# Kernel optimization log

Hardware: AMD Instinct MI355X
Metric: run time of the kernel (lower is better)

## Reference

```python
import jax, jax.numpy as jnp
import numpy as np

B, H, W, C, NH = 128, 14, 14, 768, 12
HD = C // NH  # 64
L = 2 * H - 1  # 27, rel pos table length


def setup_inputs() -> dict:
    key = jax.random.key(0)
    ks = jax.random.split(key, 6)
    return {
        "hidden_states": jax.random.normal(ks[0], (B, H, W, C), jnp.float32),
        "w_qkv": jax.random.normal(ks[1], (C, 3 * C), jnp.float32) * 0.02,
        "b_qkv": jnp.zeros((3 * C,), jnp.float32),
        "rel_pos_h": jax.random.normal(ks[2], (L, HD), jnp.float32) * 0.02,
        "rel_pos_w": jax.random.normal(ks[3], (L, HD), jnp.float32) * 0.02,
        "w_proj": jax.random.normal(ks[4], (C, C), jnp.float32) * 0.02,
        "b_proj": jnp.zeros((C,), jnp.float32),
    }


def _rel_table(size, rel_pos):
    # q_size == k_size -> coords = q - k + (size - 1), pure gather (no resize)
    coords = jnp.arange(size)[:, None] - jnp.arange(size)[None, :] + (size - 1)
    return rel_pos[coords]  # (size, size, HD)


def reference(hidden_states, w_qkv, b_qkv, rel_pos_h, rel_pos_w, w_proj, b_proj):
    scale = HD ** -0.5
    x = hidden_states.reshape(B, H * W, C)
    qkv = x @ w_qkv + b_qkv                                    # (B, HW, 3C)
    qkv = qkv.reshape(B, H * W, 3, NH, HD)
    qkv = jnp.transpose(qkv, (2, 0, 3, 1, 4)).reshape(3, B * NH, H * W, HD)
    q, k, v = qkv[0], qkv[1], qkv[2]                           # (B*NH, HW, HD)

    attn = jnp.einsum('bqd,bkd->bqk', q * scale, k)            # (B*NH, HW, HW)

    Rh = _rel_table(H, rel_pos_h)                              # (H, H, HD)
    Rw = _rel_table(W, rel_pos_w)                              # (W, W, HD)
    qr = q.reshape(B * NH, H, W, HD)
    rel_h = jnp.einsum('bhwc,hkc->bhwk', qr, Rh)               # (B*NH, H, W, H)
    rel_w = jnp.einsum('bhwc,wkc->bhwk', qr, Rw)               # (B*NH, H, W, W)

    attn = attn.reshape(B * NH, H, W, H, W)
    attn = attn + rel_h[..., :, None] + rel_w[..., None, :]
    attn = attn.reshape(B * NH, H * W, H * W)
    attn = jax.nn.softmax(attn, axis=-1)

    out = attn @ v                                             # (B*NH, HW, HD)
    out = out.reshape(B, NH, H, W, HD)
    out = jnp.transpose(out, (0, 2, 3, 1, 4)).reshape(B, H, W, C)
    return out @ w_proj + b_proj
```

## Files before the change

kernel.cpp:

```cpp
#include <hip/hip_runtime.h>

typedef __bf16 bf16_t;
typedef __bf16 bf16x4 __attribute__((ext_vector_type(4)));
typedef __bf16 bf16x8 __attribute__((ext_vector_type(8)));
typedef float floatx4 __attribute__((ext_vector_type(4)));

#define B_    128
#define H_    14
#define HW_   196
#define C_    768
#define NH_   12
#define HD_   64
#define M_    25088
#define NQKV_ 2304
#define KDIM_ 768
#define BK_   64
#define NKT_  12
#define VPAD_ 208
#define RSTR  72
#define QSTR  104
#define PSTR  232

__device__ __forceinline__ void async_cp16(const void* g, void* l) {
    __builtin_amdgcn_global_load_lds((const __attribute__((address_space(1))) void*)g,
                                     (__attribute__((address_space(3))) void*)l, 16, 0, 0);
}

__global__ __launch_bounds__(256) void cast_x_kernel(const float* __restrict__ in,
                                                     bf16_t* __restrict__ out) {
    size_t i = ((size_t)blockIdx.x * 256 + threadIdx.x) * 8;
    float4 a = *(const float4*)(in + i);
    float4 b = *(const float4*)(in + i + 4);
    bf16x8 v;
    v[0] = (bf16_t)a.x; v[1] = (bf16_t)a.y; v[2] = (bf16_t)a.z; v[3] = (bf16_t)a.w;
    v[4] = (bf16_t)b.x; v[5] = (bf16_t)b.y; v[6] = (bf16_t)b.z; v[7] = (bf16_t)b.w;
    *(bf16x8*)(out + i) = v;
}

__global__ __launch_bounds__(256) void zero_vpad_kernel(bf16_t* __restrict__ vtb) {
    int row = blockIdx.x * 256 + threadIdx.x;
    if (row < B_ * NH_ * HD_) {
        bf16_t* p = vtb + (size_t)row * VPAD_ + HW_;
        #pragma unroll
        for (int i = 0; i < 12; i++) p[i] = (bf16_t)0.f;
    }
}

__global__ __launch_bounds__(256) void transpose_cast_kernel(const float* __restrict__ in,
                                                             bf16_t* __restrict__ out,
                                                             int rows, int cols) {
    __shared__ float tile[32][33];
    int c0 = blockIdx.x * 32, r0 = blockIdx.y * 32;
    for (int i = threadIdx.y; i < 32; i += 8) {
        int r = r0 + i, c = c0 + threadIdx.x;
        if (r < rows && c < cols) tile[i][threadIdx.x] = in[(size_t)r * cols + c];
    }
    __syncthreads();
    for (int i = threadIdx.y; i < 32; i += 8) {
        int orow = c0 + i;
        int oc   = r0 + threadIdx.x;
        if (orow < cols && oc < rows)
            out[(size_t)orow * rows + oc] = (bf16_t)tile[threadIdx.x][i];
    }
}

__device__ __forceinline__ void stage128(const bf16_t* __restrict__ G, int g0, int kt,
                                         bf16_t (*Lb)[BK_], int tid) {
    const int sr = tid >> 3, cc = tid & 7;
    #pragma unroll
    for (int i = 0; i < 4; i++) {
        int row  = sr + i * 32;
        int scol = ((cc ^ (row & 7)) * 8);
        async_cp16(G + (size_t)(g0 + row) * KDIM_ + kt * BK_ + scol, &Lb[row][cc * 8]);
    }
}

__device__ __forceinline__ void gemm128_pipe(const bf16_t* __restrict__ A,
                                             const bf16_t* __restrict__ Bt,
                                             int m0, int n0,
                                             floatx4 acc[4][4],
                                             bf16_t (*As)[BK_], bf16_t (*Bs)[BK_]) {
    const int tid  = threadIdx.x;
    const int lane = tid & 63, wave = tid >> 6;
    const int wm = (wave & 1) << 6, wn = (wave >> 1) << 6;
    const int lrow = lane & 15, quad = lane >> 4;

    #pragma unroll
    for (int i = 0; i < 4; i++)
        #pragma unroll
        for (int j = 0; j < 4; j++) acc[i][j] = (floatx4){0.f, 0.f, 0.f, 0.f};

    stage128(A,  m0, 0, As, tid);
    stage128(Bt, n0, 0, Bs, tid);

    for (int kt = 0; kt < NKT_; kt++) {
        __builtin_amdgcn_sched_barrier(0);
        asm volatile("s_waitcnt vmcnt(0) lgkmcnt(0)" ::: "memory");
        __builtin_amdgcn_s_barrier();
        __builtin_amdgcn_sched_barrier(0);

        bf16_t (*Ab)[BK_] = As + (kt & 1) * 128;
        bf16_t (*Bb)[BK_] = Bs + (kt & 1) * 128;

        if (kt + 1 < NKT_) {
            stage128(A,  m0, kt + 1, As + ((kt + 1) & 1) * 128, tid);
            stage128(Bt, n0, kt + 1, Bs + ((kt + 1) & 1) * 128, tid);
        }

        #pragma unroll
        for (int kh = 0; kh < 2; kh++) {
            bf16x8 af[4], bfr[4];
            #pragma unroll
            for (int i = 0; i < 4; i++) {
                int rw = wm + i * 16 + lrow;
                af[i] = *(const bf16x8*)&Ab[rw][((kh * 4 + quad) ^ (rw & 7)) * 8];
            }
            #pragma unroll
            for (int j = 0; j < 4; j++) {
                int rw = wn + j * 16 + lrow;
                bfr[j] = *(const bf16x8*)&Bb[rw][((kh * 4 + quad) ^ (rw & 7)) * 8];
            }
            #pragma unroll
            for (int i = 0; i < 4; i++)
                #pragma unroll
                for (int j = 0; j < 4; j++)
                    acc[i][j] = __builtin_amdgcn_mfma_f32_16x16x32_bf16(af[i], bfr[j], acc[i][j], 0, 0, 0);
        }
    }
    __syncthreads();
}

__global__ __launch_bounds__(256) void qkv_gemm_kernel(const bf16_t* __restrict__ A,
                                                       const bf16_t* __restrict__ Bt,
                                                       const float* __restrict__ bias,
                                                       bf16_t* __restrict__ qb,
                                                       bf16_t* __restrict__ kb,
                                                       bf16_t* __restrict__ vtb) {
    __shared__ __align__(16) char smem[65536];
    bf16_t (*As)[BK_] = (bf16_t(*)[BK_])smem;
    bf16_t (*Bs)[BK_] = (bf16_t(*)[BK_])(smem + 32768);
    bf16_t (*Cs)[136] = (bf16_t(*)[136])smem;

    const int lin = blockIdx.x;
    const int g = lin / 72, r = lin - g * 72;
    const int m0 = (g * 4 + (r & 3)) * 128;
    const int n0 = (r >> 2) * 128;
    floatx4 acc[4][4];
    gemm128_pipe(A, Bt, m0, n0, acc, As, Bs);

    const int tid = threadIdx.x;
    const int lane = tid & 63, wave = tid >> 6;
    const int wm = (wave & 1) << 6, wn = (wave >> 1) << 6;
    const int lrow = lane & 15, quad = lane >> 4;
    const int sel = n0 / C_;

    if (sel == 2) {
        #pragma unroll
        for (int j = 0; j < 4; j++) {
            int n = n0 + wn + j * 16 + lrow;
            float bv = bias[n];
            int nc = n - 2 * C_;
            int nh = nc >> 6, hd = nc & 63;
            #pragma unroll
            for (int i = 0; i < 4; i++) {
                int m = m0 + wm + i * 16 + quad * 4;
                int b = m / HW_, t = m - b * HW_;
                int head = b * NH_ + nh;
                ushort4 pk;
                bf16_t h;
                h = (bf16_t)(acc[i][j][0] + bv); pk.x = __builtin_bit_cast(unsigned short, h);
                h = (bf16_t)(acc[i][j][1] + bv); pk.y = __builtin_bit_cast(unsigned short, h);
                h = (bf16_t)(acc[i][j][2] + bv); pk.z = __builtin_bit_cast(unsigned short, h);
                h = (bf16_t)(acc[i][j][3] + bv); pk.w = __builtin_bit_cast(unsigned short, h);
                *(ushort4*)(vtb + ((size_t)head * HD_ + hd) * VPAD_ + t) = pk;
            }
        }
    } else {
        const float sc = (sel == 0) ? 0.125f : 1.0f;
        #pragma unroll
        for (int j = 0; j < 4; j++) {
            int n = n0 + wn + j * 16 + lrow;
            float bv = bias[n];
            #pragma unroll
            for (int i = 0; i < 4; i++)
                #pragma unroll
                for (int rr = 0; rr < 4; rr++)
                    Cs[wm + i * 16 + quad * 4 + rr][wn + j * 16 + lrow] =
                        (bf16_t)((acc[i][j][rr] + bv) * sc);
        }
        __syncthreads();
        bf16_t* dst = sel ? kb : qb;
        const int n0s = n0 - sel * C_;
        #pragma unroll
        for (int u = 0; u < 8; u++) {
            int idx = tid + u * 256;
            int rr = idx >> 4, c = idx & 15;
            int m = m0 + rr;
            int b = m / HW_, t = m - b * HW_;
            int ncol = n0s + c * 8;
            int nh = ncol >> 6, hd = ncol & 63;
            *(uint4*)(dst + (((size_t)(b * NH_ + nh)) * HW_ + t) * HD_ + hd) =
                *(const uint4*)&Cs[rr][c * 8];
        }
    }
}

__global__ __launch_bounds__(256) void proj_gemm_kernel(const bf16_t* __restrict__ A,
                                                        const bf16_t* __restrict__ Bt,
                                                        const float* __restrict__ bias,
                                                        float* __restrict__ out) {
    __shared__ __align__(16) bf16_t As[256][BK_];
    __shared__ __align__(16) bf16_t Bs[256][BK_];
    const int lin = blockIdx.x;
    const int g = lin / 24, r = lin - g * 24;
    const int m0 = (g * 4 + (r & 3)) * 128;
    const int n0 = (r >> 2) * 128;
    floatx4 acc[4][4];
    gemm128_pipe(A, Bt, m0, n0, acc, As, Bs);

    const int lane = threadIdx.x & 63, wave = threadIdx.x >> 6;
    const int wm = (wave & 1) << 6, wn = (wave >> 1) << 6;
    const int lrow = lane & 15, quad = lane >> 4;
    #pragma unroll
    for (int j = 0; j < 4; j++) {
        int n = n0 + wn + j * 16 + lrow;
        float bv = bias[n];
        #pragma unroll
        for (int i = 0; i < 4; i++) {
            #pragma unroll
            for (int rr = 0; rr < 4; rr++) {
                int m = m0 + wm + i * 16 + quad * 4 + rr;
                out[(size_t)m * C_ + n] = acc[i][j][rr] + bv;
            }
        }
    }
}

__global__ __launch_bounds__(256, 2) void attn_kernel(const bf16_t* __restrict__ qb,
                                                      const bf16_t* __restrict__ kb,
                                                      const bf16_t* __restrict__ vtb,
                                                      const float* __restrict__ rph,
                                                      const float* __restrict__ rpw,
                                                      bf16_t* __restrict__ aout) {
    const int head = blockIdx.x;
    const int bb = head / NH_, nh = head - bb * NH_;
    const int tid = threadIdx.x;
    const int lane = tid & 63, wave = tid >> 6;
    const int lrow = lane & 15, quad = lane >> 4;

    __shared__ __align__(16) bf16_t qs[32][QSTR];
    __shared__ __align__(16) bf16_t ks[208][QSTR];
    __shared__ __align__(16) bf16_t pb[32][PSTR];
    __shared__ __align__(16) bf16_t rT[64][RSTR];
    __shared__ bf16_t QRh[32][34];
    __shared__ bf16_t QRw[32][34];
    __shared__ float pmax[2][32], psum[2][32];

    bf16x8 z;
    #pragma unroll
    for (int e = 0; e < 8; e++) z[e] = (bf16_t)0.f;

    #pragma unroll
    for (int t2 = 0; t2 < 2; t2++) {
        int u = tid * 2 + t2;
        int which = u >> 8, rem = u & 255;
        int l = rem >> 3, c = (rem & 7) * 8;
        bf16x8 v = z;
        if (l < 27) {
            const float* src = (which ? rpw : rph) + (size_t)l * HD_ + c;
            float4 a = *(const float4*)src;
            float4 b = *(const float4*)(src + 4);
            v[0] = (bf16_t)a.x; v[1] = (bf16_t)a.y; v[2] = (bf16_t)a.z; v[3] = (bf16_t)a.w;
            v[4] = (bf16_t)b.x; v[5] = (bf16_t)b.y; v[6] = (bf16_t)b.z; v[7] = (bf16_t)b.w;
        }
        *(bf16x8*)&rT[which * 32 + l][c] = v;
    }
    for (int v8 = tid; v8 < 208 * 8; v8 += 256) {
        int row = v8 >> 3, col = (v8 & 7) * 8;
        *(bf16x8*)&ks[row][col] =
            (row < HW_) ? *(const bf16x8*)(kb + ((size_t)head * HW_ + row) * HD_ + col) : z;
    }
    for (int u = tid; u < 208 * 5; u += 256) {
        int row = u / 5, c = u - row * 5;
        *(bf16x8*)&ks[row][64 + c * 8] = z;
    }

    bf16x8 vfr[2][7];
    #pragma unroll
    for (int jj = 0; jj < 2; jj++) {
        int hdt = (wave >> 1) * 2 + jj;
        #pragma unroll
        for (int kk = 0; kk < 7; kk++) {
            int col = kk * 32 + quad * 8;
            bool ok = (col < VPAD_);
            bf16x8 t = *(const bf16x8*)(vtb + ((size_t)head * HD_ + hdt * 16 + lrow) * VPAD_
                                        + (ok ? col : 0));
            vfr[jj][kk] = ok ? t : z;
        }
    }

    const int qrow_st = tid >> 3, qcol_st = (tid & 7) * 8;
    bf16x8 qreg = *(const bf16x8*)(qb + ((size_t)head * HW_ + qrow_st) * HD_ + qcol_st);

    __syncthreads();
    if (tid < HW_) {
        int kh = tid / 14, kw = tid - kh * 14;
        ks[tid][64 + kh] = (bf16_t)1.0f;
        ks[tid][78 + kw] = (bf16_t)1.0f;
    }
    if (tid < 96) {
        int row = tid / 3, col = 208 + (tid % 3) * 8;
        *(bf16x8*)&pb[row][col] = z;
    }

    const int wh = wave >> 1, mi = wave & 1;
    const int qit = wave & 1;

    for (int qt = 0; qt < 7; qt++) {
        const int q0 = qt * 32;

        *(bf16x8*)&qs[qrow_st][qcol_st] = qreg;
        __syncthreads();

        #pragma unroll
        for (int t2 = 0; t2 < 2; t2++) {
            int tsk = wave * 2 + t2;
            int which = tsk >> 2, mi2 = (tsk >> 1) & 1, ni = tsk & 1;
            floatx4 a4 = (floatx4){0.f, 0.f, 0.f, 0.f};
            #pragma unroll
            for (int kk = 0; kk < 2; kk++) {
                bf16x8 af  = *(const bf16x8*)&qs[mi2 * 16 + lrow][kk * 32 + quad * 8];
                bf16x8 bf8 = *(const bf16x8*)&rT[which * 32 + ni * 16 + lrow][kk * 32 + quad * 8];
                a4 = __builtin_amdgcn_mfma_f32_16x16x32_bf16(af, bf8, a4, 0, 0, 0);
            }
            int l = ni * 16 + lrow;
            if (l < 27) {
                bf16_t (*QR)[34] = which ? QRw : QRh;
                #pragma unroll
                for (int rr = 0; rr < 4; rr++) QR[mi2 * 16 + quad * 4 + rr][l] = (bf16_t)(a4[rr] * 8.f);
            }
        }
        __syncthreads();

        {
            int row = tid >> 3;
            int kk4 = (tid & 7) * 4;
            int t = q0 + row;
            int h = t / 14, w = t - h * 14;
            bf16x4 pk;
            #pragma unroll
            for (int s = 0; s < 4; s++) {
                int kk = kk4 + s;
                bf16_t val = (bf16_t)0.f;
                if (kk < 14)      val = QRh[row][h - kk + 13];
                else if (kk < 28) val = QRw[row][w - (kk - 14) + 13];
                pk[s] = val;
            }
            *(bf16x4*)&qs[row][64 + kk4] = pk;
        }
        __syncthreads();

        float sv[7][4];
        float m4[4] = {-1e30f, -1e30f, -1e30f, -1e30f};
        #pragma unroll
        for (int t = 0; t < 7; t++) {
            int jt = 2 * t + wh;
            if (jt < 13) {
                floatx4 a4 = (floatx4){0.f, 0.f, 0.f, 0.f};
                #pragma unroll
                for (int kk = 0; kk < 3; kk++) {
                    bf16x8 af  = *(const bf16x8*)&qs[mi * 16 + lrow][kk * 32 + quad * 8];
                    bf16x8 bf8 = *(const bf16x8*)&ks[jt * 16 + lrow][kk * 32 + quad * 8];
                    a4 = __builtin_amdgcn_mfma_f32_16x16x32_bf16(af, bf8, a4, 0, 0, 0);
                }
                int n = jt * 16 + lrow;
                bool valid = (n < HW_);
                #pragma unroll
                for (int rr = 0; rr < 4; rr++) {
                    float s = valid ? a4[rr] : -1e30f;
                    sv[t][rr] = s;
                    m4[rr] = fmaxf(m4[rr], s);
                }
            }
        }
        #pragma unroll
        for (int off = 1; off < 16; off <<= 1)
            #pragma unroll
            for (int rr = 0; rr < 4; rr++) m4[rr] = fmaxf(m4[rr], __shfl_xor(m4[rr], off));
        if (lrow == 0)
            #pragma unroll
            for (int rr = 0; rr < 4; rr++) pmax[wh][mi * 16 + quad * 4 + rr] = m4[rr];
        __syncthreads();

        float mxr[4], s4[4] = {0.f, 0.f, 0.f, 0.f};
        #pragma unroll
        for (int rr = 0; rr < 4; rr++) {
            int qi = mi * 16 + quad * 4 + rr;
            mxr[rr] = fmaxf(pmax[0][qi], pmax[1][qi]);
        }
        #pragma unroll
        for (int t = 0; t < 7; t++) {
            int jt = 2 * t + wh;
            if (jt < 13) {
                int n = jt * 16 + lrow;
                #pragma unroll
                for (int rr = 0; rr < 4; rr++) {
                    float e = __expf(sv[t][rr] - mxr[rr]);
                    s4[rr] += e;
                    pb[mi * 16 + quad * 4 + rr][n] = (bf16_t)e;
                }
            }
        }
        #pragma unroll
        for (int off = 1; off < 16; off <<= 1)
            #pragma unroll
            for (int rr = 0; rr < 4; rr++) s4[rr] += __shfl_xor(s4[rr], off);
        if (lrow == 0)
            #pragma unroll
            for (int rr = 0; rr < 4; rr++) psum[wh][mi * 16 + quad * 4 + rr] = s4[rr];
        __syncthreads();

        const int qrow = qit * 16 + lrow;
        const float inv = 1.f / (psum[0][qrow] + psum[1][qrow]);
        const int t_out = q0 + qrow;

        if (qt < 6) {
            int t = q0 + 32 + qrow_st;
            qreg = (t < HW_) ? *(const bf16x8*)(qb + ((size_t)head * HW_ + t) * HD_ + qcol_st) : z;
        }

        #pragma unroll
        for (int jj = 0; jj < 2; jj++) {
            int hdt = (wave >> 1) * 2 + jj;
            floatx4 a4 = (floatx4){0.f, 0.f, 0.f, 0.f};
            #pragma unroll
            for (int kk = 0; kk < 7; kk++) {
                bf16x8 bf8 = *(const bf16x8*)&pb[qit * 16 + lrow][kk * 32 + quad * 8];
                a4 = __builtin_amdgcn_mfma_f32_16x16x32_bf16(vfr[jj][kk], bf8, a4, 0, 0, 0);
            }
            if (t_out < HW_) {
                int col = nh * HD_ + hdt * 16 + quad * 4;
                ushort4 pk;
                bf16_t hv;
                hv = (bf16_t)(a4[0] * inv); pk.x = __builtin_bit_cast(unsigned short, hv);
                hv = (bf16_t)(a4[1] * inv); pk.y = __builtin_bit_cast(unsigned short, hv);
                hv = (bf16_t)(a4[2] * inv); pk.z = __builtin_bit_cast(unsigned short, hv);
                hv = (bf16_t)(a4[3] * inv); pk.w = __builtin_bit_cast(unsigned short, hv);
                *(ushort4*)(aout + ((size_t)bb * HW_ + t_out) * C_ + col) = pk;
            }
        }
    }
}

extern "C" void kernel_launch(void* const* d_in, const int* in_sizes, int n_in,
                              void* d_out, int out_size, void* d_ws, size_t ws_size,
                              hipStream_t stream) {
    const float* hs    = (const float*)d_in[0];
    const float* wqkv  = (const float*)d_in[1];
    const float* bqkv  = (const float*)d_in[2];
    const float* rph   = (const float*)d_in[3];
    const float* rpw   = (const float*)d_in[4];
    const float* wproj = (const float*)d_in[5];
    const float* bproj = (const float*)d_in[6];
    float* out = (float*)d_out;

    char* ws = (char*)d_ws;
    bf16_t* x_bf   = (bf16_t*)(ws + 0);
    bf16_t* aout   = x_bf;
    bf16_t* wqkvT  = (bf16_t*)(ws + 38535168);
    bf16_t* wprojT = (bf16_t*)(ws + 42074112);
    bf16_t* qb     = (bf16_t*)(ws + 43253760);
    bf16_t* kb     = (bf16_t*)(ws + 81788928);
    bf16_t* vtb    = (bf16_t*)(ws + 120324096);

    cast_x_kernel<<<9408, 256, 0, stream>>>(hs, x_bf);
    zero_vpad_kernel<<<384, 256, 0, stream>>>(vtb);
    transpose_cast_kernel<<<dim3(72, 24), dim3(32, 8), 0, stream>>>(wqkv, wqkvT, 768, 2304);
    transpose_cast_kernel<<<dim3(24, 24), dim3(32, 8), 0, stream>>>(wproj, wprojT, 768, 768);
    qkv_gemm_kernel<<<3528, 256, 0, stream>>>(x_bf, wqkvT, bqkv, qb, kb, vtb);
    attn_kernel<<<B_ * NH_, 256, 0, stream>>>(qb, kb, vtb, rph, rpw, aout);
    proj_gemm_kernel<<<1176, 256, 0, stream>>>(aout, wprojT, bproj, out);
}
```

Measured before the change: 413.1 us.

## Restructure QKV GEMM into 256x256 tiles with 8-wave ping-pong pipeline

Rewrites the QKV projection GEMM to use 256x256 output tiles per 512-thread block. Each block has a double-buffered 128KB LDS staging area, and the A and B tile loads are split across phases so they overlap with MFMA bursts under barriers and setprio. The epilogue writes the tile through LDS in two column halves. Larger tiles raise arithmetic intensity and cut global re-reads, at the cost of 128KB LDS per block, heavy register use and fewer blocks. The diff also inserts a dead dummy LDS read into gemm128_pipe, which is still used by the proj GEMM.

Measured after the change: 404.8 us. 2.0% less time.

```diff
diff --git a/kernel.cpp b/kernel.cpp
--- a/kernel.cpp
+++ b/kernel.cpp
@@ -75,6 +75,17 @@
     }
 }
 
+__device__ __forceinline__ void stage256(const bf16_t* __restrict__ G, int g0, int kt,
+                                         bf16_t (*Lb)[BK_], int tid) {
+    #pragma unroll
+    for (int r = 0; r < 4; r++) {
+        int idx = r * 512 + tid;
+        int row = idx >> 3, cc = idx & 7;
+        int scol = (cc ^ (row & 7)) * 8;
+        async_cp16(G + (size_t)(g0 + row) * KDIM_ + kt * BK_ + scol, &Lb[row][cc * 8]);
+    }
+}
+
 __device__ __forceinline__ void gemm128_pipe(const bf16_t* __restrict__ A,
                                              const bf16_t* __restrict__ Bt,
                                              int m0, int n0,
@@ -118,6 +129,11 @@
             #pragma unroll
             for (int j = 0; j < 4; j++) {
                 int rw = wn + j * 16 + lrow;
+                bfr[j] = *(const bf16x8*)&Bs[0][0];
+            }
+            #pragma unroll
+            for (int j = 0; j < 4; j++) {
+                int rw = wn + j * 16 + lrow;
                 bfr[j] = *(const bf16x8*)&Bb[rw][((kh * 4 + quad) ^ (rw & 7)) * 8];
             }
             #pragma unroll
@@ -130,40 +146,141 @@
     __syncthreads();
 }
 
-__global__ __launch_bounds__(256) void qkv_gemm_kernel(const bf16_t* __restrict__ A,
-                                                       const bf16_t* __restrict__ Bt,
-                                                       const float* __restrict__ bias,
-                                                       bf16_t* __restrict__ qb,
-                                                       bf16_t* __restrict__ kb,
-                                                       bf16_t* __restrict__ vtb) {
-    __shared__ __align__(16) char smem[65536];
-    bf16_t (*As)[BK_] = (bf16_t(*)[BK_])smem;
-    bf16_t (*Bs)[BK_] = (bf16_t(*)[BK_])(smem + 32768);
-    bf16_t (*Cs)[136] = (bf16_t(*)[136])smem;
-
-    const int lin = blockIdx.x;
-    const int g = lin / 72, r = lin - g * 72;
-    const int m0 = (g * 4 + (r & 3)) * 128;
-    const int n0 = (r >> 2) * 128;
-    floatx4 acc[4][4];
-    gemm128_pipe(A, Bt, m0, n0, acc, As, Bs);
-
-    const int tid = threadIdx.x;
+__global__ __launch_bounds__(512, 2) void qkv_gemm_kernel(const bf16_t* __restrict__ A,
+                                                          const bf16_t* __restrict__ Bt,
+                                                          const float* __restrict__ bias,
+                                                          bf16_t* __restrict__ qb,
+                                                          bf16_t* __restrict__ kb,
+                                                          bf16_t* __restrict__ vtb) {
+    __shared__ __align__(16) char smem[131072];
+    bf16_t (*AbAll)[256][64] = (bf16_t(*)[256][64])smem;
+    bf16_t (*BbAll)[256][64] = (bf16_t(*)[256][64])(smem + 65536);
+    bf16_t (*Cs)[136]        = (bf16_t(*)[136])smem;
+
+    const int tid  = threadIdx.x;
     const int lane = tid & 63, wave = tid >> 6;
-    const int wm = (wave & 1) << 6, wn = (wave >> 1) << 6;
+    const int wr = wave >> 2, wc = wave & 3;
     const int lrow = lane & 15, quad = lane >> 4;
+    const int c0 = ((quad ^ (lrow & 7)) * 8);
+    const int c1 = (((4 + quad) ^ (lrow & 7)) * 8);
+
+    const int bm = blockIdx.x / 9, bn = blockIdx.x % 9;
+    const int m0 = bm * 256, n0 = bn * 256;
+
+    floatx4 acc[8][4];
+    #pragma unroll
+    for (int i = 0; i < 8; i++)
+        #pragma unroll
+        for (int j = 0; j < 4; j++) acc[i][j] = (floatx4){0.f, 0.f, 0.f, 0.f};
+
+    stage256(A,  m0, 0, AbAll[0], tid);
+    stage256(Bt, n0, 0, BbAll[0], tid);
+    asm volatile("s_waitcnt vmcnt(0)" ::: "memory");
+    __builtin_amdgcn_s_barrier();
+    __builtin_amdgcn_sched_barrier(0);
+
+    for (int kt = 0; kt < NKT_; kt++) {
+        bf16_t (*Ab)[64] = AbAll[kt & 1];
+        bf16_t (*Bb)[64] = BbAll[kt & 1];
+        const int arow = wr * 128 + lrow;
+        const int brow = wc * 64 + lrow;
+
+        bf16x8 af[4][2], bfA[2][2], bfB[2][2];
+
+        #pragma unroll
+        for (int i = 0; i < 4; i++) {
+            af[i][0] = *(const bf16x8*)&Ab[arow + i * 16][c0];
+            af[i][1] = *(const bf16x8*)&Ab[arow + i * 16][c1];
+        }
+        #pragma unroll
+        for (int j = 0; j < 2; j++) {
+            bfA[j][0] = *(const bf16x8*)&Bb[brow + j * 16][c0];
+            bfA[j][1] = *(const bf16x8*)&Bb[brow + j * 16][c1];
+        }
+        if (kt < NKT_ - 1) stage256(A, m0, kt + 1, AbAll[(kt + 1) & 1], tid);
+        __builtin_amdgcn_s_barrier();
+        asm volatile("s_waitcnt lgkmcnt(0)" ::: "memory");
+        __builtin_amdgcn_sched_barrier(0);
+        __builtin_amdgcn_s_setprio(1);
+        #pragma unroll
+        for (int i = 0; i < 4; i++)
+            #pragma unroll
+            for (int j = 0; j < 2; j++) {
+                acc[i][j] = __builtin_amdgcn_mfma_f32_16x16x32_bf16(af[i][0], bfA[j][0], acc[i][j], 0, 0, 0);
+                acc[i][j] = __builtin_amdgcn_mfma_f32_16x16x32_bf16(af[i][1], bfA[j][1], acc[i][j], 0, 0, 0);
+            }
+        __builtin_amdgcn_s_setprio(0);
+        __builtin_amdgcn_sched_barrier(0);
+        __builtin_amdgcn_s_barrier();
+
+        #pragma unroll
+        for (int j = 0; j < 2; j++) {
+            bfB[j][0] = *(const bf16x8*)&Bb[brow + 32 + j * 16][c0];
+            bfB[j][1] = *(const bf16x8*)&Bb[brow + 32 + j * 16][c1];
+        }
+        if (kt < NKT_ - 1) stage256(Bt, n0, kt + 1, BbAll[(kt + 1) & 1], tid);
+        __builtin_amdgcn_s_barrier();
+        asm volatile("s_waitcnt lgkmcnt(0)" ::: "memory");
+        __builtin_amdgcn_sched_barrier(0);
+        __builtin_amdgcn_s_setprio(1);
+        #pragma unroll
+        for (int i = 0; i < 4; i++)
+            #pragma unroll
+            for (int j = 0; j < 2; j++) {
+                acc[i][2 + j] = __builtin_amdgcn_mfma_f32_16x16x32_bf16(af[i][0], bfB[j][0], acc[i][2 + j], 0, 0, 0);
+                acc[i][2 + j] = __builtin_amdgcn_mfma_f32_16x16x32_bf16(af[i][1], bfB[j][1], acc[i][2 + j], 0, 0, 0);
+            }
+        __builtin_amdgcn_s_setprio(0);
+        __builtin_amdgcn_sched_barrier(0);
+        __builtin_amdgcn_s_barrier();
+
+        #pragma unroll
+        for (int i = 0; i < 4; i++) {
+            af[i][0] = *(const bf16x8*)&Ab[arow + 64 + i * 16][c0];
+            af[i][1] = *(const bf16x8*)&Ab[arow + 64 + i * 16][c1];
+        }
+        __builtin_amdgcn_s_barrier();
+        asm volatile("s_waitcnt lgkmcnt(0)" ::: "memory");
+        __builtin_amdgcn_sched_barrier(0);
+        __builtin_amdgcn_s_setprio(1);
+        #pragma unroll
+        for (int i = 0; i < 4; i++)
+            #pragma unroll
+            for (int j = 0; j < 2; j++) {
+                acc[4 + i][j] = __builtin_amdgcn_mfma_f32_16x16x32_bf16(af[i][0], bfA[j][0], acc[4 + i][j], 0, 0, 0);
+                acc[4 + i][j] = __builtin_amdgcn_mfma_f32_16x16x32_bf16(af[i][1], bfA[j][1], acc[4 + i][j], 0, 0, 0);
+            }
+        __builtin_amdgcn_s_setprio(0);
+        __builtin_amdgcn_sched_barrier(0);
+        __builtin_amdgcn_s_barrier();
+
+        __builtin_amdgcn_s_setprio(1);
+        #pragma unroll
+        for (int i = 0; i < 4; i++)
+            #pragma unroll
+            for (int j = 0; j < 2; j++) {
+                acc[4 + i][2 + j] = __builtin_amdgcn_mfma_f32_16x16x32_bf16(af[i][0], bfB[j][0], acc[4 + i][2 + j], 0, 0, 0);
+                acc[4 + i][2 + j] = __builtin_amdgcn_mfma_f32_16x16x32_bf16(af[i][1], bfB[j][1], acc[4 + i][2 + j], 0, 0, 0);
+            }
+        __builtin_amdgcn_s_setprio(0);
+        __builtin_amdgcn_sched_barrier(0);
+        asm volatile("s_waitcnt vmcnt(0)" ::: "memory");
+        __builtin_amdgcn_s_barrier();
+        __builtin_amdgcn_sched_barrier(0);
+    }
+
     const int sel = n0 / C_;
 
     if (sel == 2) {
         #pragma unroll
         for (int j = 0; j < 4; j++) {
-            int n = n0 + wn + j * 16 + lrow;
+            int n = n0 + wc * 64 + j * 16 + lrow;
             float bv = bias[n];
             int nc = n - 2 * C_;
             int nh = nc >> 6, hd = nc & 63;
             #pragma unroll
-            for (int i = 0; i < 4; i++) {
-                int m = m0 + wm + i * 16 + quad * 4;
+            for (int i = 0; i < 8; i++) {
+                int m = m0 + wr * 128 + i * 16 + quad * 4;
                 int b = m / HW_, t = m - b * HW_;
                 int head = b * NH_ + nh;
                 ushort4 pk;
@@ -177,30 +294,37 @@
         }
     } else {
         const float sc = (sel == 0) ? 0.125f : 1.0f;
-        #pragma unroll
-        for (int j = 0; j < 4; j++) {
-            int n = n0 + wn + j * 16 + lrow;
-            float bv = bias[n];
-            #pragma unroll
-            for (int i = 0; i < 4; i++)
-                #pragma unroll
-                for (int rr = 0; rr < 4; rr++)
-                    Cs[wm + i * 16 + quad * 4 + rr][wn + j * 16 + lrow] =
-                        (bf16_t)((acc[i][j][rr] + bv) * sc);
-        }
-        __syncthreads();
         bf16_t* dst = sel ? kb : qb;
         const int n0s = n0 - sel * C_;
         #pragma unroll
-        for (int u = 0; u < 8; u++) {
-            int idx = tid + u * 256;
-            int rr = idx >> 4, c = idx & 15;
-            int m = m0 + rr;
-            int b = m / HW_, t = m - b * HW_;
-            int ncol = n0s + c * 8;
-            int nh = ncol >> 6, hd = ncol & 63;
-            *(uint4*)(dst + (((size_t)(b * NH_ + nh)) * HW_ + t) * HD_ + hd) =
-                *(const uint4*)&Cs[rr][c * 8];
+        for (int hh = 0; hh < 2; hh++) {
+            __syncthreads();
+            if ((wc >> 1) == hh) {
+                #pragma unroll
+                for (int j = 0; j < 4; j++) {
+                    int n = n0 + wc * 64 + j * 16 + lrow;
+                    float bv = bias[n];
+                    int ccol = (wc & 1) * 64 + j * 16 + lrow;
+                    #pragma unroll
+                    for (int i = 0; i < 8; i++)
+                        #pragma unroll
+                        for (int rr = 0; rr < 4; rr++)
+                            Cs[wr * 128 + i * 16 + quad * 4 + rr][ccol] =
+                                (bf16_t)((acc[i][j][rr] + bv) * sc);
+                }
+            }
+            __syncthreads();
+            #pragma unroll
+            for (int u = 0; u < 8; u++) {
+                int idx = tid + u * 512;
+                int rr = idx >> 4, c = idx & 15;
+                int m = m0 + rr;
+                int b = m / HW_, t = m - b * HW_;
+                int ncol = n0s + hh * 128 + c * 8;
+                int nh = ncol >> 6, hd = ncol & 63;
+                *(uint4*)(dst + (((size_t)(b * NH_ + nh)) * HW_ + t) * HD_ + hd) =
+                    *(const uint4*)&Cs[rr][c * 8];
+            }
         }
     }
 }
@@ -477,7 +601,7 @@
     zero_vpad_kernel<<<384, 256, 0, stream>>>(vtb);
     transpose_cast_kernel<<<dim3(72, 24), dim3(32, 8), 0, stream>>>(wqkv, wqkvT, 768, 2304);
     transpose_cast_kernel<<<dim3(24, 24), dim3(32, 8), 0, stream>>>(wproj, wprojT, 768, 768);
-    qkv_gemm_kernel<<<3528, 256, 0, stream>>>(x_bf, wqkvT, bqkv, qb, kb, vtb);
+    qkv_gemm_kernel<<<98 * 9, 512, 0, stream>>>(x_bf, wqkvT, bqkv, qb, kb, vtb);
     attn_kernel<<<B_ * NH_, 256, 0, stream>>>(qb, kb, vtb, rph, rpw, aout);
     proj_gemm_kernel<<<1176, 256, 0, stream>>>(aout, wprojT, bproj, out);
 }
```
